# Optimization experiments

Hardware: AMD Instinct MI355X
Metric: run time of the kernel (lower is better)

The kernel has to match this reference:

```python
import jax, jax.numpy as jnp
import numpy as np

MIN_EXPERTS = 1
MAX_EXPERTS = 8
TEMPERATURE = 1.0


def setup_inputs() -> dict:
    key = jax.random.key(0)
    ks = jax.random.split(key, 7)
    B, S, H, E = 8, 4096, 1024, 64
    Hh = H // 2
    return {
        "hidden_states": jax.random.normal(ks[0], (B, S, H), dtype=jnp.float32),
        "W_router": jax.random.normal(ks[1], (E, H), dtype=jnp.float32) * 0.02,
        "b_router": jax.random.normal(ks[2], (E,), dtype=jnp.float32) * 0.02,
        "W1": jax.random.normal(ks[3], (Hh, H), dtype=jnp.float32) * 0.02,
        "b1": jax.random.normal(ks[4], (Hh,), dtype=jnp.float32) * 0.02,
        "W2": jax.random.normal(ks[5], (1, Hh), dtype=jnp.float32) * 0.02,
        "b2": jax.random.normal(ks[6], (1,), dtype=jnp.float32) * 0.02,
    }


def reference(hidden_states, W_router, b_router, W1, b1, W2, b2):
    B, S, H = hidden_states.shape
    flat = hidden_states.reshape(-1, H)                     # [N, H]

    # router logits
    router_logits = (flat @ W_router.T + b_router) / TEMPERATURE  # [N, E]

    # confidence net: Linear -> ReLU -> Linear -> Sigmoid
    h = jax.nn.relu(flat @ W1.T + b1)                       # [N, H/2]
    confidence = jax.nn.sigmoid(h @ W2.T + b2).squeeze(-1)  # [N]

    # dynamic k per token (torch.round = half-to-even, same as jnp.round)
    dk = MIN_EXPERTS + (MAX_EXPERTS - MIN_EXPERTS) * (1.0 - confidence)
    dk = jnp.clip(jnp.round(dk), MIN_EXPERTS, MAX_EXPERTS).astype(jnp.int32)  # [N]

    routing_probs = jax.nn.softmax(router_logits, axis=-1)  # [N, E]

    # single top-k pass replaces per-iteration sort; mask slots >= dynamic_k
    top_vals, top_idx = jax.lax.top_k(routing_probs, MAX_EXPERTS)  # [N, max_k]
    slot = jnp.arange(MAX_EXPERTS, dtype=jnp.int32)[None, :]       # [1, max_k]
    active = slot < dk[:, None]                                    # [N, max_k]
    sel_w = jnp.where(active, top_vals, 0.0)
    sel_i = jnp.where(active, top_idx, 0).astype(jnp.int64)

    sel_w = sel_w.reshape(B, S, MAX_EXPERTS)
    sel_i = sel_i.reshape(B, S, MAX_EXPERTS)
    return sel_w, sel_i, confidence, router_logits
```

## Files before the change

### kernel.cpp

```cpp
#include <hip/hip_runtime.h>
#include <hip/hip_bf16.h>
#include <math.h>

#define N_TOK 32768
#define HDIM 1024
#define HH 512
#define NOUT 576
#define BM 256
#define BN 64
#define BK 32
#define THREADS 256
#define KC 384

#define OFF_SELW 0
#define OFF_SELI 262144
#define OFF_CONF 524288
#define OFF_LOG  557056

__device__ float  g_Bmat[HDIM * NOUT];
__device__ double g_partial[N_TOK * 8];

__global__ __launch_bounds__(256) void k_build(const float* __restrict__ W1,
                                               const float* __restrict__ Wr) {
  int idx = blockIdx.x * 256 + threadIdx.x;
  int k = idx / NOUT;
  int j = idx - k * NOUT;
  float v = (j < HH) ? W1[(size_t)j * HDIM + k] : Wr[(size_t)(j - HH) * HDIM + k];
  g_Bmat[idx] = v;
}

__global__ __launch_bounds__(THREADS, 2) void k_gemm(const float* __restrict__ A,
                                                     const float* __restrict__ b1,
                                                     const float* __restrict__ W2,
                                                     const float* __restrict__ b_router,
                                                     float* __restrict__ out_logits) {
  __shared__ float As[2][BK][BM];
  __shared__ float Bs[2][BK][BN];

  int bid = blockIdx.x;
  int xcd = bid & 7;
  int s   = bid >> 3;
  int j   = s % 9;
  int t   = xcd + 8 * (s / 9);

  const int tid = threadIdx.x;
  const int tx  = tid & 7;
  const int ty  = tid >> 3;
  const int m0  = t * BM;
  const int n0  = j * BN;

  float acc[8][8];
  float carry[8][8];
  #pragma unroll
  for (int i = 0; i < 8; ++i)
    #pragma unroll
    for (int c = 0; c < 8; ++c) { acc[i][c] = 0.f; carry[i][c] = 0.f; }

  const float* Ag = A + (size_t)(m0 + tid) * HDIM;

  float4 av[8];
  float4 bv[2];

  #pragma unroll
  for (int c = 0; c < 8; ++c) av[c] = *(const float4*)(Ag + c * 4);
  #pragma unroll
  for (int c = 0; c < 2; ++c) {
    int g  = tid + c * 256;
    int kr = g >> 4;
    int ch = g & 15;
    bv[c] = *(const float4*)&g_Bmat[(size_t)kr * NOUT + n0 + ch * 4];
  }
  #pragma unroll
  for (int c = 0; c < 8; ++c) {
    int kb = c * 4;
    As[0][kb + 0][tid] = av[c].x;
    As[0][kb + 1][tid] = av[c].y;
    As[0][kb + 2][tid] = av[c].z;
    As[0][kb + 3][tid] = av[c].w;
  }
  #pragma unroll
  for (int c = 0; c < 2; ++c) {
    int g  = tid + c * 256;
    int kr = g >> 4;
    int ch = g & 15;
    *(float4*)&Bs[0][kr][ch * 4] = bv[c];
  }
  __syncthreads();

  int p = 0;
  for (int k0 = 0; k0 < HDIM; k0 += BK) {
    const bool not_last = (k0 + BK < HDIM);

    if (not_last) {
      #pragma unroll
      for (int c = 0; c < 8; ++c) av[c] = *(const float4*)(Ag + (k0 + BK) + c * 4);
      #pragma unroll
      for (int c = 0; c < 2; ++c) {
        int g  = tid + c * 256;
        int kr = g >> 4;
        int ch = g & 15;
        bv[c] = *(const float4*)&g_Bmat[(size_t)(k0 + BK + kr) * NOUT + n0 + ch * 4];
      }
    }

    if (k0 == KC || k0 == 2 * KC) {
      #pragma unroll
      for (int i = 0; i < 8; ++i)
        #pragma unroll
        for (int c = 0; c < 8; ++c) {
          carry[i][c] = carry[i][c] + acc[i][c];
          acc[i][c] = 0.f;
        }
    }

    #pragma unroll 2
    for (int kk = 0; kk < BK; ++kk) {
      float4 a03 = *(const float4*)&As[p][kk][ty * 8 + 0];
      float4 a47 = *(const float4*)&As[p][kk][ty * 8 + 4];
      float4 b03 = *(const float4*)&Bs[p][kk][tx * 8 + 0];
      float4 b47 = *(const float4*)&Bs[p][kk][tx * 8 + 4];
      float a[8] = {a03.x, a03.y, a03.z, a03.w, a47.x, a47.y, a47.z, a47.w};
      float b[8] = {b03.x, b03.y, b03.z, b03.w, b47.x, b47.y, b47.z, b47.w};
      #pragma unroll
      for (int i = 0; i < 8; ++i)
        #pragma unroll
        for (int c = 0; c < 8; ++c)
          acc[i][c] = fmaf(a[i], b[c], acc[i][c]);
    }

    if (not_last) {
      #pragma unroll
      for (int c = 0; c < 8; ++c) {
        int kb = c * 4;
        As[p ^ 1][kb + 0][tid] = av[c].x;
        As[p ^ 1][kb + 1][tid] = av[c].y;
        As[p ^ 1][kb + 2][tid] = av[c].z;
        As[p ^ 1][kb + 3][tid] = av[c].w;
      }
      #pragma unroll
      for (int c = 0; c < 2; ++c) {
        int g  = tid + c * 256;
        int kr = g >> 4;
        int ch = g & 15;
        *(float4*)&Bs[p ^ 1][kr][ch * 4] = bv[c];
      }
      __syncthreads();
      p ^= 1;
    }
  }

  #pragma unroll
  for (int i = 0; i < 8; ++i)
    #pragma unroll
    for (int c = 0; c < 8; ++c) carry[i][c] = carry[i][c] + acc[i][c];

  if (j < 8) {
    double w2v[8];
    float  b1v[8];
    #pragma unroll
    for (int c = 0; c < 8; ++c) {
      w2v[c] = (double)W2[n0 + tx * 8 + c];
      b1v[c] = b1[n0 + tx * 8 + c];
    }
    #pragma unroll
    for (int i = 0; i < 8; ++i) {
      double sacc = 0.0;
      #pragma unroll
      for (int c = 0; c < 8; ++c) {
        float h = fmaxf(carry[i][c] + b1v[c], 0.f);
        sacc = fma((double)h, w2v[c], sacc);
      }
      sacc += __shfl_xor(sacc, 1, 64);
      sacc += __shfl_xor(sacc, 2, 64);
      sacc += __shfl_xor(sacc, 4, 64);
      if (tx == 0) g_partial[(size_t)(m0 + ty * 8 + i) * 8 + j] = sacc;
    }
  } else {
    float brv[8];
    #pragma unroll
    for (int c = 0; c < 8; ++c) brv[c] = b_router[tx * 8 + c];
    #pragma unroll
    for (int i = 0; i < 8; ++i) {
      int row = m0 + ty * 8 + i;
      float o[8];
      #pragma unroll
      for (int c = 0; c < 8; ++c) o[c] = carry[i][c] + brv[c];
      *(float4*)&out_logits[(size_t)row * 64 + tx * 8 + 0] =
          make_float4(o[0], o[1], o[2], o[3]);
      *(float4*)&out_logits[(size_t)row * 64 + tx * 8 + 4] =
          make_float4(o[4], o[5], o[6], o[7]);
    }
  }
}

__global__ __launch_bounds__(256) void k_post(const float* __restrict__ b2,
                                              float* __restrict__ d_out) {
  const int lane = threadIdx.x & 63;
  const int wave = threadIdx.x >> 6;
  const int q    = lane & 7;
  const int tsub = lane >> 3;
  const int tk   = blockIdx.x * 32 + wave * 8 + tsub;

  double p = g_partial[(size_t)tk * 8 + q];
  p += __shfl_xor(p, 1, 64);
  p += __shfl_xor(p, 2, 64);
  p += __shfl_xor(p, 4, 64);
  double ca   = (double)b2[0] + p;
  double conf = 1.0 / (1.0 + exp(-ca));
  double dkf  = 1.0 + 7.0 * (1.0 - conf);
  double dkr  = rint(dkf);
  int dk = (int)fmin(fmax(dkr, 1.0), 8.0);

  const float* logits = d_out + OFF_LOG + (size_t)tk * 64;
  float l[8];
  #pragma unroll
  for (int b = 0; b < 8; ++b) l[b] = logits[b * 8 + q];

  float mx = l[0];
  #pragma unroll
  for (int b = 1; b < 8; ++b) mx = fmaxf(mx, l[b]);
  mx = fmaxf(mx, __shfl_xor(mx, 1, 64));
  mx = fmaxf(mx, __shfl_xor(mx, 2, 64));
  mx = fmaxf(mx, __shfl_xor(mx, 4, 64));

  float ex[8];
  #pragma unroll
  for (int b = 0; b < 8; ++b) ex[b] = expf(l[b] - mx);

  float r = ex[0];
  #pragma unroll
  for (int b = 1; b < 8; ++b) r += ex[b];
  r += __shfl_xor(r, 1, 64);
  r += __shfl_xor(r, 2, 64);
  float ssum = r + __shfl_xor(r, 4, 64);

  float v[8];
  #pragma unroll
  for (int b = 0; b < 8; ++b) v[b] = ex[b] / ssum;

  float myw = 0.f, myi = 0.f;
  unsigned used = 0u;
  #pragma unroll
  for (int slot = 0; slot < 8; ++slot) {
    float best = -1.f;
    int   bi   = 64;
    #pragma unroll
    for (int b = 0; b < 8; ++b) {
      bool ok = (((used >> b) & 1u) == 0u) && (v[b] > best);
      best = ok ? v[b] : best;
      bi   = ok ? (b * 8 + q) : bi;
    }
    #pragma unroll
    for (int m = 1; m <= 4; m <<= 1) {
      float ow = __shfl_xor(best, m, 64);
      int   oi = __shfl_xor(bi,   m, 64);
      bool take = (ow > best) || (ow == best && oi < bi);
      best = take ? ow : best;
      bi   = take ? oi : bi;
    }
    if ((bi & 7) == q) used |= (1u << (bi >> 3));
    bool active = slot < dk;
    if (slot == q) {
      myw = active ? best : 0.f;
      myi = active ? (float)bi : 0.f;
    }
  }

  d_out[OFF_SELW + (size_t)tk * 8 + q] = myw;
  d_out[OFF_SELI + (size_t)tk * 8 + q] = myi;
  if (q == 0) d_out[OFF_CONF + tk] = (float)conf;
}

extern "C" void kernel_launch(void* const* d_in, const int* in_sizes, int n_in,
                              void* d_out, int out_size, void* d_ws, size_t ws_size,
                              hipStream_t stream) {
  const float* hidden   = (const float*)d_in[0];
  const float* W_router = (const float*)d_in[1];
  const float* b_router = (const float*)d_in[2];
  const float* W1       = (const float*)d_in[3];
  const float* b1       = (const float*)d_in[4];
  const float* W2       = (const float*)d_in[5];
  const float* b2       = (const float*)d_in[6];
  float* out = (float*)d_out;

  k_build<<<(HDIM * NOUT) / 256, 256, 0, stream>>>(W1, W_router);
  k_gemm<<<(N_TOK / BM) * 9, THREADS, 0, stream>>>(hidden, b1, W2, b_router,
                                                   out + OFF_LOG);
  k_post<<<N_TOK / 32, 256, 0, stream>>>(b2, out);
}
```

Measured before the change: 727.1 us.

## Stage GEMM tiles directly to LDS with global_load_lds and swizzled A layout

Replaces the register-staged double buffer in the fused router/confidence GEMM with `__builtin_amdgcn_global_load_lds` 16-byte async copies straight into shared memory. The A tile is stored row-major with an XOR swizzle on its column chunks, so per-k fragments can be read as float4 with fewer bank conflicts. The block shrinks to 128 threads and BM=128, doubling the grid. The aim is to cut VGPR pressure and the transpose-store work of the old staging, at the cost of relying on the compiler to place the wait before the barrier and of lower per-block data reuse.

```diff
diff --git a/kernel.cpp b/kernel.cpp
--- a/kernel.cpp
+++ b/kernel.cpp
@@ -6,10 +6,10 @@
 #define HDIM 1024
 #define HH 512
 #define NOUT 576
-#define BM 256
+#define BM 128
 #define BN 64
 #define BK 32
-#define THREADS 256
+#define THREADS 128
 #define KC 384
 
 #define OFF_SELW 0
@@ -17,7 +17,7 @@
 #define OFF_CONF 524288
 #define OFF_LOG  557056
 
-__device__ float  g_Bmat[HDIM * NOUT];
+__device__ __align__(16) float  g_Bmat[HDIM * NOUT];
 __device__ double g_partial[N_TOK * 8];
 
 __global__ __launch_bounds__(256) void k_build(const float* __restrict__ W1,
@@ -29,13 +29,19 @@
   g_Bmat[idx] = v;
 }
 
+__device__ __forceinline__ void gl_lds16(const float* g, float* l) {
+  __builtin_amdgcn_global_load_lds(
+      (const __attribute__((address_space(1))) void*)g,
+      (__attribute__((address_space(3))) void*)l, 16, 0, 0);
+}
+
 __global__ __launch_bounds__(THREADS, 2) void k_gemm(const float* __restrict__ A,
                                                      const float* __restrict__ b1,
                                                      const float* __restrict__ W2,
                                                      const float* __restrict__ b_router,
                                                      float* __restrict__ out_logits) {
-  __shared__ float As[2][BK][BM];
-  __shared__ float Bs[2][BK][BN];
+  __shared__ __align__(16) float As[2][BM][BK];
+  __shared__ __align__(16) float Bs[2][BK][BN];
 
   int bid = blockIdx.x;
   int xcd = bid & 7;
@@ -43,11 +49,19 @@
   int j   = s % 9;
   int t   = xcd + 8 * (s / 9);
 
-  const int tid = threadIdx.x;
-  const int tx  = tid & 7;
-  const int ty  = tid >> 3;
-  const int m0  = t * BM;
-  const int n0  = j * BN;
+  const int tid  = threadIdx.x;
+  const int lane = tid & 63;
+  const int w    = tid >> 6;
+  const int tx   = tid & 7;
+  const int ty   = tid >> 3;
+  const int ty7  = ty & 7;
+  const int m0   = t * BM;
+  const int n0   = j * BN;
+
+  const int a_r  = lane >> 3;
+  const int a_c4 = (lane & 7) * 4;
+  const int b_r  = lane >> 4;
+  const int b_c4 = (lane & 15) * 4;
 
   float acc[8][8];
   float carry[8][8];
@@ -56,52 +70,28 @@
     #pragma unroll
     for (int c = 0; c < 8; ++c) { acc[i][c] = 0.f; carry[i][c] = 0.f; }
 
-  const float* Ag = A + (size_t)(m0 + tid) * HDIM;
-
-  float4 av[8];
-  float4 bv[2];
-
-  #pragma unroll
-  for (int c = 0; c < 8; ++c) av[c] = *(const float4*)(Ag + c * 4);
-  #pragma unroll
-  for (int c = 0; c < 2; ++c) {
-    int g  = tid + c * 256;
-    int kr = g >> 4;
-    int ch = g & 15;
-    bv[c] = *(const float4*)&g_Bmat[(size_t)kr * NOUT + n0 + ch * 4];
-  }
-  #pragma unroll
-  for (int c = 0; c < 8; ++c) {
-    int kb = c * 4;
-    As[0][kb + 0][tid] = av[c].x;
-    As[0][kb + 1][tid] = av[c].y;
-    As[0][kb + 2][tid] = av[c].z;
-    As[0][kb + 3][tid] = av[c].w;
-  }
-  #pragma unroll
-  for (int c = 0; c < 2; ++c) {
-    int g  = tid + c * 256;
-    int kr = g >> 4;
-    int ch = g & 15;
-    *(float4*)&Bs[0][kr][ch * 4] = bv[c];
-  }
+  auto stage = [&](int pb, int k0) {
+    #pragma unroll
+    for (int ci = 0; ci < 8; ++ci) {
+      int sg = w * 8 + ci;
+      const float* src = A + (size_t)(m0 + sg * 8 + a_r) * HDIM + k0 +
+                         (a_c4 ^ ((sg & 7) * 4));
+      gl_lds16(src, &As[pb][0][0] + sg * 256);
+    }
+    #pragma unroll
+    for (int ci = 0; ci < 4; ++ci) {
+      int sg = w * 4 + ci;
+      const float* src = g_Bmat + (size_t)(k0 + sg * 4 + b_r) * NOUT + n0 + b_c4;
+      gl_lds16(src, &Bs[pb][0][0] + sg * 256);
+    }
+  };
+
+  stage(0, 0);
   __syncthreads();
 
   int p = 0;
   for (int k0 = 0; k0 < HDIM; k0 += BK) {
-    const bool not_last = (k0 + BK < HDIM);
-
-    if (not_last) {
-      #pragma unroll
-      for (int c = 0; c < 8; ++c) av[c] = *(const float4*)(Ag + (k0 + BK) + c * 4);
-      #pragma unroll
-      for (int c = 0; c < 2; ++c) {
-        int g  = tid + c * 256;
-        int kr = g >> 4;
-        int ch = g & 15;
-        bv[c] = *(const float4*)&g_Bmat[(size_t)(k0 + BK + kr) * NOUT + n0 + ch * 4];
-      }
-    }
+    if (k0 + BK < HDIM) stage(p ^ 1, k0 + BK);
 
     if (k0 == KC || k0 == 2 * KC) {
       #pragma unroll
@@ -114,39 +104,31 @@
     }
 
     #pragma unroll 2
-    for (int kk = 0; kk < BK; ++kk) {
-      float4 a03 = *(const float4*)&As[p][kk][ty * 8 + 0];
-      float4 a47 = *(const float4*)&As[p][kk][ty * 8 + 4];
-      float4 b03 = *(const float4*)&Bs[p][kk][tx * 8 + 0];
-      float4 b47 = *(const float4*)&Bs[p][kk][tx * 8 + 4];
-      float a[8] = {a03.x, a03.y, a03.z, a03.w, a47.x, a47.y, a47.z, a47.w};
-      float b[8] = {b03.x, b03.y, b03.z, b03.w, b47.x, b47.y, b47.z, b47.w};
+    for (int kk4 = 0; kk4 < 8; ++kk4) {
+      float4 af[8];
       #pragma unroll
       for (int i = 0; i < 8; ++i)
+        af[i] = *(const float4*)&As[p][ty * 8 + i][(kk4 ^ ty7) * 4];
+      #pragma unroll
+      for (int d = 0; d < 4; ++d) {
+        float4 b03 = *(const float4*)&Bs[p][kk4 * 4 + d][tx * 8 + 0];
+        float4 b47 = *(const float4*)&Bs[p][kk4 * 4 + d][tx * 8 + 4];
+        float bb[8] = {b03.x, b03.y, b03.z, b03.w, b47.x, b47.y, b47.z, b47.w};
+        float aa[8];
         #pragma unroll
-        for (int c = 0; c < 8; ++c)
-          acc[i][c] = fmaf(a[i], b[c], acc[i][c]);
-    }
-
-    if (not_last) {
-      #pragma unroll
-      for (int c = 0; c < 8; ++c) {
-        int kb = c * 4;
-        As[p ^ 1][kb + 0][tid] = av[c].x;
-        As[p ^ 1][kb + 1][tid] = av[c].y;
-        As[p ^ 1][kb + 2][tid] = av[c].z;
-        As[p ^ 1][kb + 3][tid] = av[c].w;
+        for (int i = 0; i < 8; ++i)
+          aa[i] = (d == 0) ? af[i].x : (d == 1) ? af[i].y
+                : (d == 2) ? af[i].z : af[i].w;
+        #pragma unroll
+        for (int i = 0; i < 8; ++i)
+          #pragma unroll
+          for (int c = 0; c < 8; ++c)
+            acc[i][c] = fmaf(aa[i], bb[c], acc[i][c]);
       }
-      #pragma unroll
-      for (int c = 0; c < 2; ++c) {
-        int g  = tid + c * 256;
-        int kr = g >> 4;
-        int ch = g & 15;
-        *(float4*)&Bs[p ^ 1][kr][ch * 4] = bv[c];
-      }
-      __syncthreads();
-      p ^= 1;
-    }
+    }
+
+    __syncthreads();
+    p ^= 1;
   }
 
   #pragma unroll
```

Measured after the change: 707.1 us. -2.8%, faster.
